# Performance work log

Measured on AMD Instinct MI355X. Metric: run time of the kernel, lower is better.

## Reference

```python
import jax, jax.numpy as jnp
import numpy as np

N = 20000      # nodes per snapshot
E = 320000     # directed edges per snapshot (self-loops added in reference)
T = 8          # snapshot sequence length
IN = 1         # in_dim
H = 32         # hidden_dim
HEADS = 2      # heads in first GAT layer
EPS = 1e-16    # PyG softmax denominator epsilon


def setup_inputs() -> dict:
    key = jax.random.key(0)
    ks = jax.random.split(key, 20)
    s = 0.1  # weight scale for numerical sanity
    return {
        "x": jax.random.normal(ks[0], (T, N, IN), jnp.float32),
        "edge_index": jax.random.randint(ks[1], (T, 2, E), 0, N, jnp.int64),
        # GAT layer 1: in=1 -> heads=2, out=32 (concat -> 64)
        "W1": jax.random.normal(ks[2], (IN, HEADS * H), jnp.float32) * s,
        "att_src1": jax.random.normal(ks[3], (HEADS, H), jnp.float32) * s,
        "att_dst1": jax.random.normal(ks[4], (HEADS, H), jnp.float32) * s,
        "b1": jax.random.normal(ks[5], (HEADS * H,), jnp.float32) * s,
        # GAT layer 2: in=64 -> heads=1, out=32
        "W2": jax.random.normal(ks[6], (HEADS * H, H), jnp.float32) * s,
        "att_src2": jax.random.normal(ks[7], (1, H), jnp.float32) * s,
        "att_dst2": jax.random.normal(ks[8], (1, H), jnp.float32) * s,
        "b2": jax.random.normal(ks[9], (H,), jnp.float32) * s,
        # GRU (torch layout: rows ordered r,z,n)
        "gru_w_ih": jax.random.normal(ks[10], (3 * H, H), jnp.float32) * s,
        "gru_w_hh": jax.random.normal(ks[11], (3 * H, H), jnp.float32) * s,
        "gru_b_ih": jax.random.normal(ks[12], (3 * H,), jnp.float32) * s,
        "gru_b_hh": jax.random.normal(ks[13], (3 * H,), jnp.float32) * s,
        # output head
        "fc_w": jax.random.normal(ks[14], (1, H), jnp.float32) * s,
        "fc_b": jax.random.normal(ks[15], (1,), jnp.float32) * s,
    }


def _gat_layer(x, src, dst, W, att_src, att_dst, bias, heads, dh):
    """PyG GATConv (shared src/dst lin, leaky_relu 0.2, per-dest softmax, concat heads)."""
    h = (x @ W).reshape(N, heads, dh)                      # [N,Hd,D]
    a_src = jnp.sum(h * att_src, axis=-1)                  # [N,Hd]
    a_dst = jnp.sum(h * att_dst, axis=-1)                  # [N,Hd]
    e = jax.nn.leaky_relu(a_src[src] + a_dst[dst], 0.2)    # [Eh,Hd]
    m = jax.ops.segment_max(e, dst, num_segments=N)        # per-dest max (stable)
    ex = jnp.exp(e - m[dst])
    denom = jax.ops.segment_sum(ex, dst, num_segments=N)
    alpha = ex / (denom[dst] + EPS)                        # [Eh,Hd]
    msg = h[src] * alpha[..., None]                        # [Eh,Hd,D]
    out = jax.ops.segment_sum(msg, dst, num_segments=N)    # [N,Hd,D]
    return out.reshape(N, heads * dh) + bias


def _encode(x_t, ei_t, W1, att_src1, att_dst1, b1, W2, att_src2, att_dst2, b2):
    loops = jnp.arange(N, dtype=ei_t.dtype)                # GATConv add_self_loops=True
    src = jnp.concatenate([ei_t[0], loops])
    dst = jnp.concatenate([ei_t[1], loops])
    h = jax.nn.elu(_gat_layer(x_t, src, dst, W1, att_src1, att_dst1, b1, HEADS, H))
    h = jax.nn.elu(_gat_layer(h, src, dst, W2, att_src2, att_dst2, b2, 1, H))
    return h                                                # [N,H]


def reference(x, edge_index, W1, att_src1, att_dst1, b1, W2, att_src2, att_dst2, b2,
              gru_w_ih, gru_w_hh, gru_b_ih, gru_b_hh, fc_w, fc_b):
    enc = jax.vmap(lambda xt, et: _encode(xt, et, W1, att_src1, att_dst1, b1,
                                          W2, att_src2, att_dst2, b2))(x, edge_index)  # [T,N,H]

    def gru_step(h, x_t):
        gi = x_t @ gru_w_ih.T + gru_b_ih                   # [N,3H]
        gh = h @ gru_w_hh.T + gru_b_hh
        ir, iz, in_ = jnp.split(gi, 3, axis=-1)
        hr, hz, hn = jnp.split(gh, 3, axis=-1)
        r = jax.nn.sigmoid(ir + hr)
        z = jax.nn.sigmoid(iz + hz)
        n = jnp.tanh(in_ + r * hn)
        h_new = (1.0 - z) * n + z * h
        return h_new, None

    h0 = jnp.zeros((N, H), enc.dtype)
    h_last, _ = jax.lax.scan(gru_step, h0, enc)            # last timestep hidden [N,H]
    pred = h_last @ fc_w.T + fc_b                          # [N,1]
    return pred
```

## Files before the change

kernel.cpp:

```cpp
#include <hip/hip_runtime.h>
#include <cmath>

#define NN 20000
#define NE 320000
#define TT 8
#define EPSF 1e-16f
#define NR 32
#define RSZ 625
#define NCH 1250

#define OFF_RT  0
#define OFF_ROW 1024
#define OFF_CSR (OFF_ROW + TT*(NN+1))
#define OFF_H2S (OFF_CSR + TT*NE/2)
#define OFF_AS2 (OFF_H2S + TT*NN*32)
#define OFF_AD2 (OFF_AS2 + TT*NN)
#define OFF_ENC (OFF_AD2 + TT*NN)
#define WS_WORDS (OFF_ENC + TT*NN*32)

__device__ __forceinline__ float fexp(float x) { return __expf(x); }
__device__ __forceinline__ float fsigmoid(float x) { return 1.f / (1.f + __expf(-x)); }
__device__ __forceinline__ float ftanh(float x) {
    float ax = fabsf(x);
    float e2 = __expf(-2.f * ax);
    float th = (1.f - e2) / (1.f + e2);
    return copysignf(th, x);
}

__global__ __launch_bounds__(256) void k_bhist(const int* __restrict__ ei,
                                               int* __restrict__ bh) {
    int b = blockIdx.x;
    int t = b & 7, c = b >> 3;
    __shared__ int cnt[NR];
    int tid = threadIdx.x;
    if (tid < NR) cnt[tid] = 0;
    __syncthreads();
    int e = c * 256 + tid;
    int dst = ei[(size_t)t * 2 * NE + NE + e];
    int r = dst / RSZ;
    atomicAdd(&cnt[r], 1);
    __syncthreads();
    if (tid < NR) bh[(t * NCH + c) * NR + tid] = cnt[tid];
}

__global__ __launch_bounds__(256) void k_bscan1(int* __restrict__ bh,
                                                int* __restrict__ rt) {
    int b = blockIdx.x;
    int t = b & 7, r = b >> 3;
    __shared__ int sums[256];
    int tid = threadIdx.x;
    int c0 = tid * 5, c1 = c0 + 5; if (c1 > NCH) c1 = NCH; if (c0 > NCH) c0 = NCH;
    int v[5]; int s = 0;
    for (int c = c0, k = 0; c < c1; c++, k++) { v[k] = bh[(t * NCH + c) * NR + r]; s += v[k]; }
    sums[tid] = s;
    __syncthreads();
    if (tid == 0) {
        int acc = 0;
        for (int i = 0; i < 256; i++) { int x = sums[i]; sums[i] = acc; acc += x; }
        rt[t * NR + r] = acc;
    }
    __syncthreads();
    int acc = sums[tid];
    for (int c = c0, k = 0; c < c1; c++, k++) { bh[(t * NCH + c) * NR + r] = acc; acc += v[k]; }
}

__global__ __launch_bounds__(256) void k_bplace(const int* __restrict__ ei,
                                                const int* __restrict__ bh,
                                                const int* __restrict__ rt,
                                                unsigned* __restrict__ bkt) {
    int b = blockIdx.x;
    int t = b & 7, c = b >> 3;
    __shared__ int cnt[NR], base[NR], rbs[NR];
    int tid = threadIdx.x;
    if (tid == 0) {
        int acc = 0;
        for (int r = 0; r < NR; r++) { rbs[r] = acc; acc += rt[t * NR + r]; }
    }
    if (tid < NR) {
        cnt[tid] = 0;
        base[tid] = bh[(t * NCH + c) * NR + tid];
    }
    __syncthreads();
    int e = c * 256 + tid;
    int src = ei[(size_t)t * 2 * NE + e];
    int dst = ei[(size_t)t * 2 * NE + NE + e];
    int r = dst / RSZ;
    int pos = atomicAdd(&cnt[r], 1);
    bkt[(size_t)t * NE + rbs[r] + base[r] + pos] =
        ((unsigned)src << 10) | (unsigned)(dst - r * RSZ);
}

__global__ __launch_bounds__(256) void k_csr(const unsigned* __restrict__ bkt,
                                             const int* __restrict__ rt,
                                             int* __restrict__ row,
                                             unsigned short* __restrict__ csr) {
    int b = blockIdx.x;
    int t = b & 7, r = b >> 3;
    __shared__ int segs[2];
    __shared__ int deg[RSZ];
    __shared__ int cur[RSZ];
    __shared__ int sums[256];
    int tid = threadIdx.x;
    if (tid == 0) {
        int acc = 0, s0 = 0;
        for (int i = 0; i < NR; i++) { if (i == r) s0 = acc; acc += rt[t * NR + i]; }
        segs[0] = s0;
        segs[1] = (r == NR - 1) ? acc : s0 + rt[t * NR + r];
    }
    for (int i = tid; i < RSZ; i += 256) deg[i] = 0;
    __syncthreads();
    int seg0 = segs[0], seg1 = segs[1];
    int lo = r * RSZ;
    const unsigned* bp = bkt + (size_t)t * NE;
    for (int i = seg0 + tid; i < seg1; i += 256)
        atomicAdd(&deg[bp[i] & 1023], 1);
    __syncthreads();
    int c0 = tid * 3, c1 = c0 + 3; if (c1 > RSZ) c1 = RSZ; if (c0 > RSZ) c0 = RSZ;
    int v[3]; int s = 0;
    for (int i = c0, k = 0; i < c1; i++, k++) { v[k] = deg[i]; s += v[k]; }
    sums[tid] = s;
    __syncthreads();
    if (tid == 0) {
        int acc = 0;
        for (int i = 0; i < 256; i++) { int x = sums[i]; sums[i] = acc; acc += x; }
    }
    __syncthreads();
    int acc = sums[tid];
    for (int i = c0, k = 0; i < c1; i++, k++) {
        int off = seg0 + acc;
        row[t * (NN + 1) + lo + i] = off;
        cur[i] = off;
        acc += v[k];
    }
    if (r == NR - 1 && tid == 0) row[t * (NN + 1) + NN] = seg1;
    __syncthreads();
    unsigned short* cp = csr + (size_t)t * NE;
    for (int i = seg0 + tid; i < seg1; i += 256) {
        unsigned pk = bp[i];
        int pos = atomicAdd(&cur[pk & 1023], 1);
        cp[pos] = (unsigned short)(pk >> 10);
    }
}

__global__ __launch_bounds__(256) void k_l1(
        const float* __restrict__ x, const int* __restrict__ row,
        const unsigned short* __restrict__ csr,
        const float* __restrict__ as1, const float* __restrict__ ad1,
        const float* __restrict__ W1, const float* __restrict__ b1,
        const float* __restrict__ W2,
        const float* __restrict__ as2w, const float* __restrict__ ad2w,
        float* __restrict__ h2s, float* __restrict__ as2, float* __restrict__ ad2) {
    __shared__ float sW2[64 * 32];
    __shared__ float sW1[64], sb1[64], sas[32], sad[32], sc[4];
    int tid = threadIdx.x;
    for (int i = tid; i < 64 * 32; i += 256) sW2[i] = W2[i];
    if (tid < 64) { sW1[tid] = W1[tid]; sb1[tid] = b1[tid]; }
    if (tid < 32) { sas[tid] = as2w[tid]; sad[tid] = ad2w[tid]; }
    if (tid < 4) {
        int hd = tid & 1;
        const float* att = (tid < 2) ? as1 : ad1;
        float s = 0.f;
        for (int k = 0; k < 32; k++) s += W1[hd * 32 + k] * att[hd * 32 + k];
        sc[tid] = s;
    }
    __syncthreads();
    int b = blockIdx.x;
    int t = b & 7, chunk = b >> 3;
    int n = chunk * 256 + tid;
    if (n >= NN) return;
    int idx = t * NN + n;
    float cs0 = sc[0], cs1 = sc[1], cd0 = sc[2], cd1 = sc[3];
    float xd = x[idx];
    float v0 = xd * (cs0 + cd0); v0 = v0 > 0.f ? v0 : 0.2f * v0; float ex0 = fexp(v0);
    float v1 = xd * (cs1 + cd1); v1 = v1 > 0.f ? v1 : 0.2f * v1; float ex1 = fexp(v1);
    float den0 = ex0, den1 = ex1, S0 = ex0 * xd, S1 = ex1 * xd;
    int rs = row[t * (NN + 1) + n], re = row[t * (NN + 1) + n + 1];
    const unsigned short* cp = csr + (size_t)t * NE;
    const float* xp = x + t * NN;
    int i = rs;
    for (; i < re && (i & 3); i++) {
        int src = cp[i];
        float xs = xp[src];
        float u0 = xs * cs0 + xd * cd0; u0 = u0 > 0.f ? u0 : 0.2f * u0; float q0 = fexp(u0);
        float u1 = xs * cs1 + xd * cd1; u1 = u1 > 0.f ? u1 : 0.2f * u1; float q1 = fexp(u1);
        den0 += q0; S0 += q0 * xs;
        den1 += q1; S1 += q1 * xs;
    }
    for (; i + 4 <= re; i += 4) {
        ushort4 s4 = *(const ushort4*)(cp + i);
        float xA = xp[s4.x], xB = xp[s4.y], xC = xp[s4.z], xD = xp[s4.w];
        float uA0 = xA * cs0 + xd * cd0; uA0 = uA0 > 0.f ? uA0 : 0.2f * uA0; float qA0 = fexp(uA0);
        float uB0 = xB * cs0 + xd * cd0; uB0 = uB0 > 0.f ? uB0 : 0.2f * uB0; float qB0 = fexp(uB0);
        float uC0 = xC * cs0 + xd * cd0; uC0 = uC0 > 0.f ? uC0 : 0.2f * uC0; float qC0 = fexp(uC0);
        float uD0 = xD * cs0 + xd * cd0; uD0 = uD0 > 0.f ? uD0 : 0.2f * uD0; float qD0 = fexp(uD0);
        float uA1 = xA * cs1 + xd * cd1; uA1 = uA1 > 0.f ? uA1 : 0.2f * uA1; float qA1 = fexp(uA1);
        float uB1 = xB * cs1 + xd * cd1; uB1 = uB1 > 0.f ? uB1 : 0.2f * uB1; float qB1 = fexp(uB1);
        float uC1 = xC * cs1 + xd * cd1; uC1 = uC1 > 0.f ? uC1 : 0.2f * uC1; float qC1 = fexp(uC1);
        float uD1 = xD * cs1 + xd * cd1; uD1 = uD1 > 0.f ? uD1 : 0.2f * uD1; float qD1 = fexp(uD1);
        den0 += (qA0 + qB0) + (qC0 + qD0);
        S0 += qA0 * xA + qB0 * xB + qC0 * xC + qD0 * xD;
        den1 += (qA1 + qB1) + (qC1 + qD1);
        S1 += qA1 * xA + qB1 * xB + qC1 * xC + qD1 * xD;
    }
    for (; i < re; i++) {
        int src = cp[i];
        float xs = xp[src];
        float u0 = xs * cs0 + xd * cd0; u0 = u0 > 0.f ? u0 : 0.2f * u0; float q0 = fexp(u0);
        float u1 = xs * cs1 + xd * cd1; u1 = u1 > 0.f ? u1 : 0.2f * u1; float q1 = fexp(u1);
        den0 += q0; S0 += q0 * xs;
        den1 += q1; S1 += q1 * xs;
    }
    S0 /= (den0 + EPSF);
    S1 /= (den1 + EPSF);
    float h1[64];
#pragma unroll
    for (int d = 0; d < 64; d++) {
        float v = sW1[d] * (d < 32 ? S0 : S1) + sb1[d];
        h1[d] = v > 0.f ? v : fexp(v) - 1.f;
    }
    float a_s = 0.f, a_d = 0.f;
    float acc[32];
#pragma unroll 4
    for (int j = 0; j < 32; j++) {
        float a = 0.f;
#pragma unroll
        for (int d = 0; d < 64; d++) a += h1[d] * sW2[d * 32 + j];
        acc[j] = a;
        a_s += a * sas[j];
        a_d += a * sad[j];
    }
    float4* op = (float4*)(h2s + (size_t)idx * 32);
#pragma unroll
    for (int q = 0; q < 8; q++)
        op[q] = make_float4(acc[4 * q], acc[4 * q + 1], acc[4 * q + 2], acc[4 * q + 3]);
    as2[idx] = a_s;
    ad2[idx] = a_d;
}

__global__ __launch_bounds__(256) void k_l2(
        const int* __restrict__ row, const unsigned short* __restrict__ csr,
        const float* __restrict__ as2, const float* __restrict__ ad2,
        const float* __restrict__ h2s, const float* __restrict__ b2,
        float* __restrict__ enc) {
    int tid = threadIdx.x;
    int g = tid >> 5, lane = tid & 31;
    int b = blockIdx.x;
    int t = b & 7, chunk = b >> 3;
    int n = chunk * 8 + g;
    int pair = t * NN + n;
    int base = t * NN;
    const float* hb = h2s + (size_t)base * 32;
    float adn = ad2[pair];
    float vs = as2[pair] + adn; vs = vs > 0.f ? vs : 0.2f * vs;
    float qs = fexp(vs);
    float num = qs * hb[(size_t)n * 32 + lane];
    float den_part = 0.f;
    int rs = row[t * (NN + 1) + n], re = row[t * (NN + 1) + n + 1];
    const unsigned short* cp = csr + (size_t)t * NE;
    for (int i0 = rs; i0 < re; i0 += 32) {
        int cnt = re - i0; if (cnt > 32) cnt = 32;
        float q = 0.f; int s = 0;
        if (lane < cnt) {
            s = cp[i0 + lane];
            float a = as2[base + s];
            float u = a + adn; u = u > 0.f ? u : 0.2f * u;
            q = fexp(u);
        }
        den_part += q;
        int e = 0;
        for (; e + 2 <= cnt; e += 2) {
            float q0 = __shfl(q, e, 32);
            int   s0 = __shfl(s, e, 32);
            float q1 = __shfl(q, e + 1, 32);
            int   s1 = __shfl(s, e + 1, 32);
            num += q0 * hb[(size_t)s0 * 32 + lane];
            num += q1 * hb[(size_t)s1 * 32 + lane];
        }
        if (e < cnt) {
            float q0 = __shfl(q, e, 32);
            int   s0 = __shfl(s, e, 32);
            num += q0 * hb[(size_t)s0 * 32 + lane];
        }
    }
    float den = den_part;
#pragma unroll
    for (int off = 16; off > 0; off >>= 1) den += __shfl_xor(den, off, 32);
    den += qs;
    float ev = num / (den + EPSF) + b2[lane];
    ev = ev > 0.f ? ev : fexp(ev) - 1.f;
    enc[(size_t)pair * 32 + lane] = ev;
}

__global__ __launch_bounds__(128) void k_gru(
        const float* __restrict__ enc,
        const float* __restrict__ wih, const float* __restrict__ whh,
        const float* __restrict__ bih, const float* __restrict__ bhh,
        const float* __restrict__ fcw, const float* __restrict__ fcb,
        float* __restrict__ out) {
    __shared__ float4 wpA[32 * 32];
    __shared__ float2 wpB[32 * 32];
    __shared__ float sbih[96], sbhh[96], sfw[32];
    __shared__ float4 e4[4][32], h4[4][32];
    int tid = threadIdx.x;
    for (int i = tid; i < 1024; i += 128) {
        int k = i >> 5, j = i & 31;
        wpA[i] = make_float4(wih[j * 32 + k], wih[(32 + j) * 32 + k],
                             wih[(64 + j) * 32 + k], whh[j * 32 + k]);
        wpB[i] = make_float2(whh[(32 + j) * 32 + k], whh[(64 + j) * 32 + k]);
    }
    if (tid < 96) { sbih[tid] = bih[tid]; sbhh[tid] = bhh[tid]; }
    if (tid < 32) sfw[tid] = fcw[tid];
    int g = tid >> 5, lane = tid & 31;
    int n0 = blockIdx.x * 16 + g * 4;
    float h0 = 0.f, h1 = 0.f, h2 = 0.f, h3 = 0.f;
    h4[g][lane] = make_float4(0.f, 0.f, 0.f, 0.f);
    __syncthreads();
    float bi_r = sbih[lane], bi_z = sbih[32 + lane], bi_n = sbih[64 + lane];
    float bh_r = sbhh[lane], bh_z = sbhh[32 + lane], bh_n = sbhh[64 + lane];
    for (int t = 0; t < TT; t++) {
        const float* ep = enc + ((size_t)(t * NN + n0)) * 32 + lane;
        e4[g][lane] = make_float4(ep[0], ep[32], ep[64], ep[96]);
        __syncthreads();
        float ir0 = bi_r, ir1 = bi_r, ir2 = bi_r, ir3 = bi_r;
        float iz0 = bi_z, iz1 = bi_z, iz2 = bi_z, iz3 = bi_z;
        float in0 = bi_n, in1 = bi_n, in2 = bi_n, in3 = bi_n;
        float hr0 = bh_r, hr1 = bh_r, hr2 = bh_r, hr3 = bh_r;
        float hz0 = bh_z, hz1 = bh_z, hz2 = bh_z, hz3 = bh_z;
        float hn0 = bh_n, hn1 = bh_n, hn2 = bh_n, hn3 = bh_n;
#pragma unroll 8
        for (int k = 0; k < 32; k++) {
            float4 wa = wpA[k * 32 + lane];
            float2 wb = wpB[k * 32 + lane];
            float4 ek = e4[g][k];
            float4 hk = h4[g][k];
            ir0 += wa.x * ek.x; ir1 += wa.x * ek.y; ir2 += wa.x * ek.z; ir3 += wa.x * ek.w;
            iz0 += wa.y * ek.x; iz1 += wa.y * ek.y; iz2 += wa.y * ek.z; iz3 += wa.y * ek.w;
            in0 += wa.z * ek.x; in1 += wa.z * ek.y; in2 += wa.z * ek.z; in3 += wa.z * ek.w;
            hr0 += wa.w * hk.x; hr1 += wa.w * hk.y; hr2 += wa.w * hk.z; hr3 += wa.w * hk.w;
            hz0 += wb.x * hk.x; hz1 += wb.x * hk.y; hz2 += wb.x * hk.z; hz3 += wb.x * hk.w;
            hn0 += wb.y * hk.x; hn1 += wb.y * hk.y; hn2 += wb.y * hk.z; hn3 += wb.y * hk.w;
        }
        __syncthreads();
        {
            float r, z, nn_;
            r = fsigmoid(ir0 + hr0); z = fsigmoid(iz0 + hz0);
            nn_ = ftanh(in0 + r * hn0); h0 = (1.f - z) * nn_ + z * h0;
            r = fsigmoid(ir1 + hr1); z = fsigmoid(iz1 + hz1);
            nn_ = ftanh(in1 + r * hn1); h1 = (1.f - z) * nn_ + z * h1;
            r = fsigmoid(ir2 + hr2); z = fsigmoid(iz2 + hz2);
            nn_ = ftanh(in2 + r * hn2); h2 = (1.f - z) * nn_ + z * h2;
            r = fsigmoid(ir3 + hr3); z = fsigmoid(iz3 + hz3);
            nn_ = ftanh(in3 + r * hn3); h3 = (1.f - z) * nn_ + z * h3;
        }
        h4[g][lane] = make_float4(h0, h1, h2, h3);
    }
    float fw = sfw[lane], fb = fcb[0];
    float v0 = h0 * fw, v1 = h1 * fw, v2 = h2 * fw, v3 = h3 * fw;
#pragma unroll
    for (int off = 16; off > 0; off >>= 1) {
        v0 += __shfl_down(v0, off, 32);
        v1 += __shfl_down(v1, off, 32);
        v2 += __shfl_down(v2, off, 32);
        v3 += __shfl_down(v3, off, 32);
    }
    if (lane == 0) {
        out[n0 + 0] = v0 + fb;
        out[n0 + 1] = v1 + fb;
        out[n0 + 2] = v2 + fb;
        out[n0 + 3] = v3 + fb;
    }
}

extern "C" void kernel_launch(void* const* d_in, const int* in_sizes, int n_in,
                              void* d_out, int out_size, void* d_ws, size_t ws_size,
                              hipStream_t stream) {
    const float* x    = (const float*)d_in[0];
    const int*   ei   = (const int*)d_in[1];
    const float* W1   = (const float*)d_in[2];
    const float* as1  = (const float*)d_in[3];
    const float* ad1  = (const float*)d_in[4];
    const float* b1   = (const float*)d_in[5];
    const float* W2   = (const float*)d_in[6];
    const float* as2w = (const float*)d_in[7];
    const float* ad2w = (const float*)d_in[8];
    const float* b2   = (const float*)d_in[9];
    const float* wih  = (const float*)d_in[10];
    const float* whh  = (const float*)d_in[11];
    const float* bih  = (const float*)d_in[12];
    const float* bhh  = (const float*)d_in[13];
    const float* fcw  = (const float*)d_in[14];
    const float* fcb  = (const float*)d_in[15];
    float* ws  = (float*)d_ws;
    float* out = (float*)d_out;

    int*            rt   = (int*)(ws + OFF_RT);
    int*            rowp = (int*)(ws + OFF_ROW);
    unsigned short* csr  = (unsigned short*)(ws + OFF_CSR);
    int*            bh   = (int*)(ws + OFF_H2S);
    unsigned*       bkt  = (unsigned*)(ws + OFF_ENC);

    k_bhist<<<TT * NCH, 256, 0, stream>>>(ei, bh);
    k_bscan1<<<TT * NR, 256, 0, stream>>>(bh, rt);
    k_bplace<<<TT * NCH, 256, 0, stream>>>(ei, bh, rt, bkt);
    k_csr<<<TT * NR, 256, 0, stream>>>(bkt, rt, rowp, csr);

    k_l1<<<TT * ((NN + 255) / 256), 256, 0, stream>>>(x, rowp, csr, as1, ad1,
                                              W1, b1, W2, as2w, ad2w,
                                              ws + OFF_H2S, ws + OFF_AS2, ws + OFF_AD2);

    k_l2<<<TT * (NN / 8), 256, 0, stream>>>(rowp, csr, ws + OFF_AS2, ws + OFF_AD2,
                                            ws + OFF_H2S, b2, ws + OFF_ENC);

    k_gru<<<NN / 16, 128, 0, stream>>>(ws + OFF_ENC, wih, whh, bih, bhh,
                                       fcw, fcb, out);
}
```

Measured before the change: 277.9 us.

## Prepack GRU weights, prefetch encodings, use wave barriers, vectorize L1 matvec

A new small kernel transposes and packs the GRU weights once per call, so each GRU block copies contiguous float4/float2 data instead of doing a strided gather. The GRU loop prefetches the next timestep's encodings into registers and swaps block-wide __syncthreads for wave barriers, since each warp only uses its own shared slices. The layer-1 64x32 matvec is reordered to an outer-product form with float4 shared reads, and attention dots are folded into the store loop. The risks are higher register pressure in k_l1 and one extra kernel launch.

```diff
diff --git a/kernel.cpp b/kernel.cpp
--- a/kernel.cpp
+++ b/kernel.cpp
@@ -16,7 +16,8 @@
 #define OFF_AS2 (OFF_H2S + TT*NN*32)
 #define OFF_AD2 (OFF_AS2 + TT*NN)
 #define OFF_ENC (OFF_AD2 + TT*NN)
-#define WS_WORDS (OFF_ENC + TT*NN*32)
+#define OFF_WP  (OFF_ENC + TT*NN*32)
+#define WS_WORDS (OFF_WP + 6144)
 
 __device__ __forceinline__ float fexp(float x) { return __expf(x); }
 __device__ __forceinline__ float fsigmoid(float x) { return 1.f / (1.f + __expf(-x)); }
@@ -25,6 +26,19 @@
     float e2 = __expf(-2.f * ax);
     float th = (1.f - e2) / (1.f + e2);
     return copysignf(th, x);
+}
+
+__global__ __launch_bounds__(256) void k_wpack(const float* __restrict__ wih,
+                                               const float* __restrict__ whh,
+                                               float* __restrict__ wp) {
+    int i = blockIdx.x * 256 + threadIdx.x;
+    if (i < 1024) {
+        int k = i >> 5, j = i & 31;
+        ((float4*)wp)[i] = make_float4(wih[j * 32 + k], wih[(32 + j) * 32 + k],
+                                       wih[(64 + j) * 32 + k], whh[j * 32 + k]);
+        ((float2*)(wp + 4096))[i] = make_float2(whh[(32 + j) * 32 + k],
+                                                whh[(64 + j) * 32 + k]);
+    }
 }
 
 __global__ __launch_bounds__(256) void k_bhist(const int* __restrict__ ei,
@@ -218,21 +232,29 @@
         float v = sW1[d] * (d < 32 ? S0 : S1) + sb1[d];
         h1[d] = v > 0.f ? v : fexp(v) - 1.f;
     }
+    float4 acc4[8];
+#pragma unroll
+    for (int q = 0; q < 8; q++) acc4[q] = make_float4(0.f, 0.f, 0.f, 0.f);
+    const float4* w4 = (const float4*)sW2;
+#pragma unroll 8
+    for (int d = 0; d < 64; d++) {
+        float hd = h1[d];
+#pragma unroll
+        for (int q = 0; q < 8; q++) {
+            float4 w = w4[d * 8 + q];
+            acc4[q].x += hd * w.x; acc4[q].y += hd * w.y;
+            acc4[q].z += hd * w.z; acc4[q].w += hd * w.w;
+        }
+    }
     float a_s = 0.f, a_d = 0.f;
-    float acc[32];
-#pragma unroll 4
-    for (int j = 0; j < 32; j++) {
-        float a = 0.f;
-#pragma unroll
-        for (int d = 0; d < 64; d++) a += h1[d] * sW2[d * 32 + j];
-        acc[j] = a;
-        a_s += a * sas[j];
-        a_d += a * sad[j];
-    }
     float4* op = (float4*)(h2s + (size_t)idx * 32);
 #pragma unroll
-    for (int q = 0; q < 8; q++)
-        op[q] = make_float4(acc[4 * q], acc[4 * q + 1], acc[4 * q + 2], acc[4 * q + 3]);
+    for (int q = 0; q < 8; q++) {
+        float4 a = acc4[q];
+        op[q] = a;
+        a_s += a.x * sas[4 * q] + a.y * sas[4 * q + 1] + a.z * sas[4 * q + 2] + a.w * sas[4 * q + 3];
+        a_d += a.x * sad[4 * q] + a.y * sad[4 * q + 1] + a.z * sad[4 * q + 2] + a.w * sad[4 * q + 3];
+    }
     as2[idx] = a_s;
     ad2[idx] = a_d;
 }
@@ -292,8 +314,7 @@
 }
 
 __global__ __launch_bounds__(128) void k_gru(
-        const float* __restrict__ enc,
-        const float* __restrict__ wih, const float* __restrict__ whh,
+        const float* __restrict__ enc, const float* __restrict__ wp,
         const float* __restrict__ bih, const float* __restrict__ bhh,
         const float* __restrict__ fcw, const float* __restrict__ fcb,
         float* __restrict__ out) {
@@ -302,12 +323,9 @@
     __shared__ float sbih[96], sbhh[96], sfw[32];
     __shared__ float4 e4[4][32], h4[4][32];
     int tid = threadIdx.x;
-    for (int i = tid; i < 1024; i += 128) {
-        int k = i >> 5, j = i & 31;
-        wpA[i] = make_float4(wih[j * 32 + k], wih[(32 + j) * 32 + k],
-                             wih[(64 + j) * 32 + k], whh[j * 32 + k]);
-        wpB[i] = make_float2(whh[(32 + j) * 32 + k], whh[(64 + j) * 32 + k]);
-    }
+    const float4* wpAg = (const float4*)wp;
+    const float2* wpBg = (const float2*)(wp + 4096);
+    for (int i = tid; i < 1024; i += 128) { wpA[i] = wpAg[i]; wpB[i] = wpBg[i]; }
     if (tid < 96) { sbih[tid] = bih[tid]; sbhh[tid] = bhh[tid]; }
     if (tid < 32) sfw[tid] = fcw[tid];
     int g = tid >> 5, lane = tid & 31;
@@ -317,17 +335,22 @@
     __syncthreads();
     float bi_r = sbih[lane], bi_z = sbih[32 + lane], bi_n = sbih[64 + lane];
     float bh_r = sbhh[lane], bh_z = sbhh[32 + lane], bh_n = sbhh[64 + lane];
+    const float* ep0 = enc + (size_t)n0 * 32 + lane;
+    float4 ecur = make_float4(ep0[0], ep0[32], ep0[64], ep0[96]);
     for (int t = 0; t < TT; t++) {
-        const float* ep = enc + ((size_t)(t * NN + n0)) * 32 + lane;
-        e4[g][lane] = make_float4(ep[0], ep[32], ep[64], ep[96]);
-        __syncthreads();
+        e4[g][lane] = ecur;
+        __builtin_amdgcn_wave_barrier();
+        if (t < TT - 1) {
+            const float* ep = enc + ((size_t)((t + 1) * NN + n0)) * 32 + lane;
+            ecur = make_float4(ep[0], ep[32], ep[64], ep[96]);
+        }
         float ir0 = bi_r, ir1 = bi_r, ir2 = bi_r, ir3 = bi_r;
         float iz0 = bi_z, iz1 = bi_z, iz2 = bi_z, iz3 = bi_z;
         float in0 = bi_n, in1 = bi_n, in2 = bi_n, in3 = bi_n;
         float hr0 = bh_r, hr1 = bh_r, hr2 = bh_r, hr3 = bh_r;
         float hz0 = bh_z, hz1 = bh_z, hz2 = bh_z, hz3 = bh_z;
         float hn0 = bh_n, hn1 = bh_n, hn2 = bh_n, hn3 = bh_n;
-#pragma unroll 8
+#pragma unroll 16
         for (int k = 0; k < 32; k++) {
             float4 wa = wpA[k * 32 + lane];
             float2 wb = wpB[k * 32 + lane];
@@ -340,7 +363,7 @@
             hz0 += wb.x * hk.x; hz1 += wb.x * hk.y; hz2 += wb.x * hk.z; hz3 += wb.x * hk.w;
             hn0 += wb.y * hk.x; hn1 += wb.y * hk.y; hn2 += wb.y * hk.z; hn3 += wb.y * hk.w;
         }
-        __syncthreads();
+        __builtin_amdgcn_wave_barrier();
         {
             float r, z, nn_;
             r = fsigmoid(ir0 + hr0); z = fsigmoid(iz0 + hz0);
@@ -353,6 +376,7 @@
             nn_ = ftanh(in3 + r * hn3); h3 = (1.f - z) * nn_ + z * h3;
         }
         h4[g][lane] = make_float4(h0, h1, h2, h3);
+        __builtin_amdgcn_wave_barrier();
     }
     float fw = sfw[lane], fb = fcb[0];
     float v0 = h0 * fw, v1 = h1 * fw, v2 = h2 * fw, v3 = h3 * fw;
@@ -398,7 +422,9 @@
     unsigned short* csr  = (unsigned short*)(ws + OFF_CSR);
     int*            bh   = (int*)(ws + OFF_H2S);
     unsigned*       bkt  = (unsigned*)(ws + OFF_ENC);
-
+    float*          wp   = ws + OFF_WP;
+
+    k_wpack<<<4, 256, 0, stream>>>(wih, whh, wp);
     k_bhist<<<TT * NCH, 256, 0, stream>>>(ei, bh);
     k_bscan1<<<TT * NR, 256, 0, stream>>>(bh, rt);
     k_bplace<<<TT * NCH, 256, 0, stream>>>(ei, bh, rt, bkt);
@@ -411,6 +437,6 @@
     k_l2<<<TT * (NN / 8), 256, 0, stream>>>(rowp, csr, ws + OFF_AS2, ws + OFF_AD2,
                                             ws + OFF_H2S, b2, ws + OFF_ENC);
 
-    k_gru<<<NN / 16, 128, 0, stream>>>(ws + OFF_ENC, wih, whh, bih, bhh,
+    k_gru<<<NN / 16, 128, 0, stream>>>(ws + OFF_ENC, wp, bih, bhh,
                                        fcw, fcb, out);
 }
```

Result: no change. 283.0 us (+1.8%).
